# Kernel optimization log

Measured on AMD Instinct MI355X. Metric: run time of the kernel, lower is better.

The kernel has to match this reference:

```python
import jax, jax.numpy as jnp
import numpy as np

D = 11           # num_classes + 1 (embedding dim)
HL = 7           # window height = 1 + 2*H_PAD
WL = 7           # window width  = 1 + 2*W_PAD
PAD = 3
MAXH, MAXW = 30, 30
FF = 64          # dim_feedforward
EPS = 1e-5       # LayerNorm eps (torch default)
PAD_VALUE = 0.0


def setup_inputs() -> dict:
    key = jax.random.key(0)
    ks = jax.random.split(key, 6)
    N, C, H, W = 1, 10, 16, 16
    s = 0.1
    return {
        "x": jax.random.uniform(ks[0], (N, C, H, W), jnp.float32),
        "Wqkv": jax.random.normal(ks[1], (3 * D, D), jnp.float32) * s,  # in_proj_weight
        "Wo": jax.random.normal(ks[2], (D, D), jnp.float32) * s,        # out_proj.weight
        "W1": jax.random.normal(ks[3], (FF, D), jnp.float32) * s,       # linear1.weight
        "W2": jax.random.normal(ks[4], (D, FF), jnp.float32) * s,       # linear2.weight
        "ln1_w": jnp.ones((D,), jnp.float32),                           # norm1.weight (bias=False)
        "ln2_w": jnp.ones((D,), jnp.float32),                           # norm2.weight (bias=False)
    }


def _layer_norm(x, w):
    m = jnp.mean(x, axis=-1, keepdims=True)
    v = jnp.mean(jnp.square(x - m), axis=-1, keepdims=True)
    return (x - m) / jnp.sqrt(v + EPS) * w


def _encoder_layer(x, Wqkv, Wo, W1, W2, ln1_w, ln2_w):
    # x: [B, S, D]; post-norm, 1 head, no biases, eval mode (dropout off)
    qkv = x @ Wqkv.T
    q, k, v = jnp.split(qkv, 3, axis=-1)
    scale = 1.0 / jnp.sqrt(jnp.float32(D))
    attn = jax.nn.softmax(jnp.einsum('bqd,bkd->bqk', q, k) * scale, axis=-1)
    sa = jnp.einsum('bqk,bkd->bqd', attn, v) @ Wo.T
    x = _layer_norm(x + sa, ln1_w)
    ff = jax.nn.relu(x @ W1.T) @ W2.T
    return _layer_norm(x + ff, ln2_w)


def reference(x, Wqkv, Wo, W1, W2, ln1_w, ln2_w):
    N, C, H, W = x.shape
    C1 = C + 1
    # mask channel: 1 in the padded border, 0 inside
    mask = jnp.pad(jnp.zeros((N, 1, H, W), x.dtype),
                   ((0, 0), (0, 0), (PAD, PAD), (PAD, PAD)), constant_values=1.0)
    xp = jnp.pad(x, ((0, 0), (0, 0), (PAD, PAD), (PAD, PAD)), constant_values=PAD_VALUE)
    xp = jnp.concatenate([xp, mask], axis=1)            # [N, C+1, H+6, W+6]
    win = jnp.stack([xp[:, :, i:i + H, j:j + W]
                     for i in range(HL) for j in range(WL)], axis=-1)  # [N, C1, H, W, 49]
    win = jnp.transpose(win, (0, 2, 3, 1, 4))           # [N, H, W, C1, 49]
    win = win.reshape(N * H * W * C1, HL, WL)
    # embed window into max_height x max_width canvas (rest = pad_value)
    canvas = jnp.full((N * H * W * C1, MAXH, MAXW), PAD_VALUE, x.dtype)
    canvas = canvas.at[:, :HL, :WL].set(win)
    seq = canvas.reshape(N * H * W, C1, MAXH * MAXW).transpose(0, 2, 1)  # [B, S=900, D=11]
    out = _encoder_layer(seq, Wqkv, Wo, W1, W2, ln1_w, ln2_w)
    return out.transpose(0, 2, 1)[:, :-1]               # [B, C, 900]
```

## Files before the change

### kernel.cpp

```cpp
#include <hip/hip_runtime.h>


#define D 11
#define NW 49
#define NR 50
#define SEQ 900
#define FFD 64
#define CIN 10
#define NB 256
#define TPB 576
#define NRD (NR * D)

__global__ __launch_bounds__(TPB) void pve_kernel(
    const float* __restrict__ gx,
    const float* __restrict__ gWqkv,
    const float* __restrict__ gWo,
    const float* __restrict__ gW1,
    const float* __restrict__ gW2,
    const float* __restrict__ gln1,
    const float* __restrict__ gln2,
    float* __restrict__ out)
{
    __shared__ float sQ[33 * D];
    __shared__ float sWo[D * D];
    __shared__ float sW1[FFD * D];
    __shared__ float sW2[D * FFD];
    __shared__ float sln1[D], sln2[D];
    __shared__ float sSeq[NR][D];
    __shared__ float sK[NW][D];
    __shared__ float sV[NW][D];
    __shared__ float sQr[NR][D];
    __shared__ float sE[NR][NW];
    __shared__ float sNum[NR][D];
    __shared__ float sDen[NR];
    __shared__ float sX1[NR][D];
    __shared__ float sX1n[NR][D];
    __shared__ float sH[NR][FFD];
    __shared__ float sY[NR][D];
    __shared__ float sR[NR][D];

    const int tid = threadIdx.x;
    const int b = blockIdx.x;
    const int h = b >> 4;
    const int w = b & 15;

    const int rd = tid;
    const int r = rd / D;
    const int d = rd - r * D;

    for (int i = tid; i < 33 * D; i += TPB) sQ[i]  = gWqkv[i];
    for (int i = tid; i < D * D;  i += TPB) sWo[i] = gWo[i];
    for (int i = tid; i < FFD * D; i += TPB) sW1[i] = gW1[i];
    for (int i = tid; i < D * FFD; i += TPB) sW2[i] = gW2[i];
    if (tid < D) { sln1[tid] = gln1[tid]; sln2[tid] = gln2[tid]; }

    if (rd < NRD) {
        float val = 0.0f;
        if (r < NW) {
            const int i = r / 7, j = r - (r / 7) * 7;
            const int y = h + i, xx = w + j;
            const bool inter = (y >= 3) && (y < 19) && (xx >= 3) && (xx < 19);
            const int base = inter ? ((y - 3) * 16 + (xx - 3)) : 0;
            if (d < CIN) val = inter ? gx[d * 256 + base] : 0.0f;
            else         val = inter ? 0.0f : 1.0f;
        }
        sSeq[r][d] = val;
    }
    __syncthreads();

    if (rd < NRD) {
        float aq = 0.f, ak = 0.f, av = 0.f;
        #pragma unroll
        for (int e = 0; e < D; ++e) {
            const float se = sSeq[r][e];
            aq += se * sQ[d * D + e];
            ak += se * sQ[(D + d) * D + e];
            av += se * sQ[(2 * D + d) * D + e];
        }
        sQr[r][d] = aq;
        if (r < NW) { sK[r][d] = ak; sV[r][d] = av; }
    }
    __syncthreads();

    {
        const float scale = rsqrtf(11.0f);
        #pragma unroll
        for (int k = 0; k < 5; ++k) {
            const int idx = tid + k * TPB;
            if (idx < NR * NW) {
                const int rr = idx / NW;
                const int tt = idx - rr * NW;
                float s = 0.f;
                #pragma unroll
                for (int e = 0; e < D; ++e) s += sQr[rr][e] * sK[tt][e];
                sE[rr][tt] = __expf(s * scale);
            }
        }
    }
    __syncthreads();

    if (rd < NRD) {
        float acc = 0.f;
        #pragma unroll
        for (int t = 0; t < NW; ++t) acc += sE[r][t] * sV[t][d];
        sNum[r][d] = acc;
        if (d == 0) {
            float den = 851.0f;
            #pragma unroll
            for (int t = 0; t < NW; ++t) den += sE[r][t];
            sDen[r] = den;
        }
    }
    __syncthreads();

    if (rd < NRD) {
        float acc = 0.f;
        #pragma unroll
        for (int e = 0; e < D; ++e) acc += sNum[r][e] * sWo[d * D + e];
        sX1[r][d] = sSeq[r][d] + acc / sDen[r];
    }
    __syncthreads();

    if (rd < NRD) {
        float row[D];
        #pragma unroll
        for (int e = 0; e < D; ++e) row[e] = sX1[r][e];
        float m = 0.f;
        #pragma unroll
        for (int e = 0; e < D; ++e) m += row[e];
        m *= (1.0f / 11.0f);
        float var = 0.f;
        #pragma unroll
        for (int e = 0; e < D; ++e) { float t = row[e] - m; var += t * t; }
        var *= (1.0f / 11.0f);
        sX1n[r][d] = (row[d] - m) * rsqrtf(var + 1e-5f) * sln1[d];
    }
    __syncthreads();

    #pragma unroll
    for (int k = 0; k < 6; ++k) {
        const int idx = tid + k * TPB;
        if (idx < NR * FFD) {
            const int rr = idx >> 6;
            const int ff = idx & 63;
            float acc = 0.f;
            #pragma unroll
            for (int e = 0; e < D; ++e) acc += sX1n[rr][e] * sW1[ff * D + e];
            sH[rr][ff] = fmaxf(acc, 0.0f);
        }
    }
    __syncthreads();

    if (rd < NRD) {
        float acc = 0.f;
        #pragma unroll
        for (int f = 0; f < FFD; ++f) acc += sH[r][f] * sW2[d * FFD + f];
        sY[r][d] = sX1n[r][d] + acc;
    }
    __syncthreads();

    if (rd < NRD) {
        float row[D];
        #pragma unroll
        for (int e = 0; e < D; ++e) row[e] = sY[r][e];
        float m = 0.f;
        #pragma unroll
        for (int e = 0; e < D; ++e) m += row[e];
        m *= (1.0f / 11.0f);
        float var = 0.f;
        #pragma unroll
        for (int e = 0; e < D; ++e) { float t = row[e] - m; var += t * t; }
        var *= (1.0f / 11.0f);
        sR[r][d] = (row[d] - m) * rsqrtf(var + 1e-5f) * sln2[d];
    }
    __syncthreads();

    float4* ob4 = (float4*)(out + b * (CIN * SEQ));
    #pragma unroll
    for (int k = 0; k < 4; ++k) {
        const int qi = tid + k * TPB;
        if (qi < 2250) {
            const int c  = qi / 225;
            const int s0 = (qi - c * 225) * 4;
            float4 v4;
            float* pv = (float*)&v4;
            #pragma unroll
            for (int u = 0; u < 4; ++u) {
                const int s = s0 + u;
                const int i = s / 30;
                const int j = s - i * 30;
                pv[u] = (i < 7 && j < 7) ? sR[i * 7 + j][c] : sR[NW][c];
            }
            ob4[qi] = v4;
        }
    }
}

extern "C" void kernel_launch(void* const* d_in, const int* in_sizes, int n_in,
                              void* d_out, int out_size, void* d_ws, size_t ws_size,
                              hipStream_t stream) {
    (void)in_sizes; (void)n_in; (void)out_size; (void)d_ws; (void)ws_size;
    const float* x    = (const float*)d_in[0];
    const float* Wqkv = (const float*)d_in[1];
    const float* Wo   = (const float*)d_in[2];
    const float* W1   = (const float*)d_in[3];
    const float* W2   = (const float*)d_in[4];
    const float* ln1  = (const float*)d_in[5];
    const float* ln2  = (const float*)d_in[6];
    pve_kernel<<<NB, TPB, 0, stream>>>(x, Wqkv, Wo, W1, W2, ln1, ln2,
                                       (float*)d_out);
}
```

Baseline: 80.71 us.

## Pad shared-memory rows to 12 floats and vectorize dot products with float4

Pads all D=11 shared rows and weight rows to 12 (zero-filled) and stores V transposed with 52-wide rows, so every inner dot product can use float4 LDS reads. The scalar 11- and 49/64-length loops become 3, 13 or 16 float4 iterations with split accumulators. This is meant to cut LDS instruction count and dependency chains. LayerNorm switches to a one-pass sum/sum-of-squares variance, which slightly changes numerics. Several extra zero-fill writes for the pad columns are added.

Result: no change. 80.08 us, median of 2 (-0.8%).

```diff
diff --git a/kernel.cpp b/kernel.cpp
--- a/kernel.cpp
+++ b/kernel.cpp
@@ -2,7 +2,9 @@
 
 
 #define D 11
+#define ROWP 12
 #define NW 49
+#define NWP 52
 #define NR 50
 #define SEQ 900
 #define FFD 64
@@ -10,6 +12,16 @@
 #define NB 256
 #define TPB 576
 #define NRD (NR * D)
+
+__device__ __forceinline__ float dot12(const float4* a, const float4* b) {
+    float4 s = make_float4(0.f, 0.f, 0.f, 0.f);
+    #pragma unroll
+    for (int i = 0; i < 3; ++i) {
+        float4 x = a[i], y = b[i];
+        s.x += x.x * y.x; s.y += x.y * y.y; s.z += x.z * y.z; s.w += x.w * y.w;
+    }
+    return s.x + s.y + s.z + s.w;
+}
 
 __global__ __launch_bounds__(TPB) void pve_kernel(
     const float* __restrict__ gx,
@@ -21,23 +33,23 @@
     const float* __restrict__ gln2,
     float* __restrict__ out)
 {
-    __shared__ float sQ[33 * D];
-    __shared__ float sWo[D * D];
-    __shared__ float sW1[FFD * D];
-    __shared__ float sW2[D * FFD];
+    __shared__ __align__(16) float sQ[33 * ROWP];
+    __shared__ __align__(16) float sWo[D * ROWP];
+    __shared__ __align__(16) float sW1[FFD * ROWP];
+    __shared__ __align__(16) float sW2[D * FFD];
     __shared__ float sln1[D], sln2[D];
-    __shared__ float sSeq[NR][D];
-    __shared__ float sK[NW][D];
-    __shared__ float sV[NW][D];
-    __shared__ float sQr[NR][D];
-    __shared__ float sE[NR][NW];
-    __shared__ float sNum[NR][D];
+    __shared__ __align__(16) float sSeq[NR][ROWP];
+    __shared__ __align__(16) float sK[NW][ROWP];
+    __shared__ __align__(16) float sVt[D][NWP];
+    __shared__ __align__(16) float sQr[NR][ROWP];
+    __shared__ __align__(16) float sE[NR][NWP];
+    __shared__ __align__(16) float sNum[NR][ROWP];
     __shared__ float sDen[NR];
-    __shared__ float sX1[NR][D];
-    __shared__ float sX1n[NR][D];
-    __shared__ float sH[NR][FFD];
-    __shared__ float sY[NR][D];
-    __shared__ float sR[NR][D];
+    __shared__ __align__(16) float sX1[NR][ROWP];
+    __shared__ __align__(16) float sX1n[NR][ROWP];
+    __shared__ __align__(16) float sH[NR][FFD];
+    __shared__ __align__(16) float sY[NR][ROWP];
+    __shared__ __align__(16) float sR[NR][ROWP];
 
     const int tid = threadIdx.x;
     const int b = blockIdx.x;
@@ -48,9 +60,18 @@
     const int r = rd / D;
     const int d = rd - r * D;
 
-    for (int i = tid; i < 33 * D; i += TPB) sQ[i]  = gWqkv[i];
-    for (int i = tid; i < D * D;  i += TPB) sWo[i] = gWo[i];
-    for (int i = tid; i < FFD * D; i += TPB) sW1[i] = gW1[i];
+    for (int i = tid; i < 33 * ROWP; i += TPB) {
+        const int rr = i / ROWP, cc = i - rr * ROWP;
+        sQ[i] = (cc < D) ? gWqkv[rr * D + cc] : 0.f;
+    }
+    for (int i = tid; i < D * ROWP; i += TPB) {
+        const int rr = i / ROWP, cc = i - rr * ROWP;
+        sWo[i] = (cc < D) ? gWo[rr * D + cc] : 0.f;
+    }
+    for (int i = tid; i < FFD * ROWP; i += TPB) {
+        const int rr = i / ROWP, cc = i - rr * ROWP;
+        sW1[i] = (cc < D) ? gW1[rr * D + cc] : 0.f;
+    }
     for (int i = tid; i < D * FFD; i += TPB) sW2[i] = gW2[i];
     if (tid < D) { sln1[tid] = gln1[tid]; sln2[tid] = gln2[tid]; }
 
@@ -65,75 +86,86 @@
             else         val = inter ? 0.0f : 1.0f;
         }
         sSeq[r][d] = val;
-    }
-    __syncthreads();
-
-    if (rd < NRD) {
-        float aq = 0.f, ak = 0.f, av = 0.f;
-        #pragma unroll
-        for (int e = 0; e < D; ++e) {
-            const float se = sSeq[r][e];
-            aq += se * sQ[d * D + e];
-            ak += se * sQ[(D + d) * D + e];
-            av += se * sQ[(2 * D + d) * D + e];
-        }
+        if (d == CIN) sSeq[r][D] = 0.f;
+    }
+    __syncthreads();
+
+    if (rd < NRD) {
+        const float4* sv = (const float4*)&sSeq[r][0];
+        const float aq = dot12(sv, (const float4*)&sQ[d * ROWP]);
+        const float ak = dot12(sv, (const float4*)&sQ[(D + d) * ROWP]);
+        const float av = dot12(sv, (const float4*)&sQ[(2 * D + d) * ROWP]);
         sQr[r][d] = aq;
-        if (r < NW) { sK[r][d] = ak; sV[r][d] = av; }
+        if (d == CIN) sQr[r][D] = 0.f;
+        if (r < NW) { sK[r][d] = ak; sVt[d][r] = av;
+                      if (d == CIN) sK[r][D] = 0.f; }
+        else { sVt[d][NW] = 0.f; sVt[d][NW + 1] = 0.f; sVt[d][NW + 2] = 0.f; }
     }
     __syncthreads();
 
     {
-        const float scale = rsqrtf(11.0f);
+        const float scale = 0.30151134457776363f;
         #pragma unroll
         for (int k = 0; k < 5; ++k) {
             const int idx = tid + k * TPB;
-            if (idx < NR * NW) {
-                const int rr = idx / NW;
-                const int tt = idx - rr * NW;
-                float s = 0.f;
-                #pragma unroll
-                for (int e = 0; e < D; ++e) s += sQr[rr][e] * sK[tt][e];
-                sE[rr][tt] = __expf(s * scale);
+            if (idx < NR * NWP) {
+                const int rr = idx / NWP;
+                const int tt = idx - rr * NWP;
+                float e = 0.f;
+                if (tt < NW) {
+                    const float s = dot12((const float4*)&sQr[rr][0],
+                                          (const float4*)&sK[tt][0]);
+                    e = __expf(s * scale);
+                }
+                sE[rr][tt] = e;
             }
         }
     }
     __syncthreads();
 
     if (rd < NRD) {
-        float acc = 0.f;
-        #pragma unroll
-        for (int t = 0; t < NW; ++t) acc += sE[r][t] * sV[t][d];
-        sNum[r][d] = acc;
-        if (d == 0) {
-            float den = 851.0f;
-            #pragma unroll
-            for (int t = 0; t < NW; ++t) den += sE[r][t];
-            sDen[r] = den;
-        }
-    }
-    __syncthreads();
-
-    if (rd < NRD) {
-        float acc = 0.f;
-        #pragma unroll
-        for (int e = 0; e < D; ++e) acc += sNum[r][e] * sWo[d * D + e];
+        const float4* ev = (const float4*)&sE[r][0];
+        const float4* vv = (const float4*)&sVt[d][0];
+        float4 an = make_float4(0.f, 0.f, 0.f, 0.f);
+        float4 ad = make_float4(0.f, 0.f, 0.f, 0.f);
+        #pragma unroll
+        for (int i = 0; i < 13; ++i) {
+            const float4 e = ev[i], v = vv[i];
+            an.x += e.x * v.x; an.y += e.y * v.y;
+            an.z += e.z * v.z; an.w += e.w * v.w;
+            ad.x += e.x; ad.y += e.y; ad.z += e.z; ad.w += e.w;
+        }
+        sNum[r][d] = an.x + an.y + an.z + an.w;
+        if (d == CIN) sNum[r][D] = 0.f;
+        if (d == 0) sDen[r] = 851.0f + ad.x + ad.y + ad.z + ad.w;
+    }
+    __syncthreads();
+
+    if (rd < NRD) {
+        const float acc = dot12((const float4*)&sNum[r][0],
+                                (const float4*)&sWo[d * ROWP]);
         sX1[r][d] = sSeq[r][d] + acc / sDen[r];
-    }
-    __syncthreads();
-
-    if (rd < NRD) {
-        float row[D];
-        #pragma unroll
-        for (int e = 0; e < D; ++e) row[e] = sX1[r][e];
-        float m = 0.f;
-        #pragma unroll
-        for (int e = 0; e < D; ++e) m += row[e];
-        m *= (1.0f / 11.0f);
-        float var = 0.f;
-        #pragma unroll
-        for (int e = 0; e < D; ++e) { float t = row[e] - m; var += t * t; }
-        var *= (1.0f / 11.0f);
-        sX1n[r][d] = (row[d] - m) * rsqrtf(var + 1e-5f) * sln1[d];
+        if (d == CIN) sX1[r][D] = 0.f;
+    }
+    __syncthreads();
+
+    if (rd < NRD) {
+        const float4* xv = (const float4*)&sX1[r][0];
+        float4 s4 = make_float4(0.f, 0.f, 0.f, 0.f);
+        float4 q4 = make_float4(0.f, 0.f, 0.f, 0.f);
+        #pragma unroll
+        for (int i = 0; i < 3; ++i) {
+            const float4 x = xv[i];
+            s4.x += x.x; s4.y += x.y; s4.z += x.z; s4.w += x.w;
+            q4.x += x.x * x.x; q4.y += x.y * x.y;
+            q4.z += x.z * x.z; q4.w += x.w * x.w;
+        }
+        const float sum = s4.x + s4.y + s4.z + s4.w;
+        const float sq  = q4.x + q4.y + q4.z + q4.w;
+        const float m   = sum * (1.0f / 11.0f);
+        const float var = sq * (1.0f / 11.0f) - m * m;
+        sX1n[r][d] = (sX1[r][d] - m) * rsqrtf(var + 1e-5f) * sln1[d];
+        if (d == CIN) sX1n[r][D] = 0.f;
     }
     __syncthreads();
 
@@ -143,35 +175,44 @@
         if (idx < NR * FFD) {
             const int rr = idx >> 6;
             const int ff = idx & 63;
-            float acc = 0.f;
-            #pragma unroll
-            for (int e = 0; e < D; ++e) acc += sX1n[rr][e] * sW1[ff * D + e];
+            const float acc = dot12((const float4*)&sX1n[rr][0],
+                                    (const float4*)&sW1[ff * ROWP]);
             sH[rr][ff] = fmaxf(acc, 0.0f);
         }
     }
     __syncthreads();
 
     if (rd < NRD) {
-        float acc = 0.f;
-        #pragma unroll
-        for (int f = 0; f < FFD; ++f) acc += sH[r][f] * sW2[d * FFD + f];
-        sY[r][d] = sX1n[r][d] + acc;
-    }
-    __syncthreads();
-
-    if (rd < NRD) {
-        float row[D];
-        #pragma unroll
-        for (int e = 0; e < D; ++e) row[e] = sY[r][e];
-        float m = 0.f;
-        #pragma unroll
-        for (int e = 0; e < D; ++e) m += row[e];
-        m *= (1.0f / 11.0f);
-        float var = 0.f;
-        #pragma unroll
-        for (int e = 0; e < D; ++e) { float t = row[e] - m; var += t * t; }
-        var *= (1.0f / 11.0f);
-        sR[r][d] = (row[d] - m) * rsqrtf(var + 1e-5f) * sln2[d];
+        const float4* hv = (const float4*)&sH[r][0];
+        const float4* wv = (const float4*)&sW2[d * FFD];
+        float4 a4 = make_float4(0.f, 0.f, 0.f, 0.f);
+        #pragma unroll
+        for (int i = 0; i < 16; ++i) {
+            const float4 hh = hv[i], ww = wv[i];
+            a4.x += hh.x * ww.x; a4.y += hh.y * ww.y;
+            a4.z += hh.z * ww.z; a4.w += hh.w * ww.w;
+        }
+        sY[r][d] = sX1n[r][d] + a4.x + a4.y + a4.z + a4.w;
+        if (d == CIN) sY[r][D] = 0.f;
+    }
+    __syncthreads();
+
+    if (rd < NRD) {
+        const float4* yv = (const float4*)&sY[r][0];
+        float4 s4 = make_float4(0.f, 0.f, 0.f, 0.f);
+        float4 q4 = make_float4(0.f, 0.f, 0.f, 0.f);
+        #pragma unroll
+        for (int i = 0; i < 3; ++i) {
+            const float4 y = yv[i];
+            s4.x += y.x; s4.y += y.y; s4.z += y.z; s4.w += y.w;
+            q4.x += y.x * y.x; q4.y += y.y * y.y;
+            q4.z += y.z * y.z; q4.w += y.w * y.w;
+        }
+        const float sum = s4.x + s4.y + s4.z + s4.w;
+        const float sq  = q4.x + q4.y + q4.z + q4.w;
+        const float m   = sum * (1.0f / 11.0f);
+        const float var = sq * (1.0f / 11.0f) - m * m;
+        sR[r][d] = (sY[r][d] - m) * rsqrtf(var + 1e-5f) * sln2[d];
     }
     __syncthreads();
 
```
